# Optimization experiments

Hardware: AMD Instinct MI355X
Metric: run time of the kernel (lower is better)

The kernel has to match this reference:

```python
import jax, jax.numpy as jnp
import numpy as np

B, L, D_IN = 2, 4096, 512
H, D_K, D_V, D_OUT = 8, 64, 64, 512


def setup_inputs() -> dict:
    key = jax.random.key(0)
    k0, k1, k2, k3, k4 = jax.random.split(key, 5)
    x = jax.random.normal(k0, (B, L, D_IN), dtype=jnp.float32)
    W_q = jax.random.uniform(k1, (H, D_IN, D_K), dtype=jnp.float32)
    W_k = jax.random.uniform(k2, (H, D_IN, D_K), dtype=jnp.float32)
    W_v = jax.random.uniform(k3, (H, D_IN, D_V), dtype=jnp.float32)
    W_o = jax.random.uniform(k4, (H, D_V, D_OUT), dtype=jnp.float32)
    return {"x": x, "W_q": W_q, "W_k": W_k, "W_v": W_v, "W_o": W_o}


def reference(x, W_q, W_k, W_v, W_o):
    # x: (b, l, d_in); projections per head -> (b, h, l, d)
    Q = jnp.einsum('hjk,blj->bhlk', W_q, x)
    K = jnp.einsum('hjk,blj->bhlk', W_k, x)
    V = jnp.einsum('hjv,blj->bhlv', W_v, x)
    # no softmax: pure bilinear attention (Q K^T) V
    scores = jnp.einsum('bhik,bhjk->bhij', Q, K)          # (b, h, l, l)
    values = jnp.einsum('bhqk,bhkv->bhqv', scores, V)     # (b, h, l, d_v)
    return jnp.einsum('hvo,bhlv->blo', W_o, values)       # (b, l, d_out)
```

## Files before the change

kernel.cpp:

```cpp
#include <hip/hip_runtime.h>
#include <cstdint>


#define BDIM 2
#define LDIM 4096
#define DIN 512
#define HDIM 8
#define DK 64
#define DV 64
#define DOUT 512
#define NS 16

using bf16_t = __bf16;
typedef __bf16 bf16x8 __attribute__((ext_vector_type(8)));
typedef float floatx4 __attribute__((ext_vector_type(4)));

__device__ __forceinline__ unsigned short f2bf(float f) {
    unsigned int u = __builtin_bit_cast(unsigned int, f);
    u += 0x7FFFu + ((u >> 16) & 1u);
    return (unsigned short)(u >> 16);
}

__device__ __forceinline__ void gld_lds16(const void* g, void* l) {
    __builtin_amdgcn_global_load_lds(
        (const __attribute__((address_space(1))) void*)g,
        (__attribute__((address_space(3))) void*)l, 16, 0, 0);
}

template <int BM, int BN, bool TRANS_OUT, int OUT_MODE>
__device__ __forceinline__ void gemm_core(const bf16_t* A, const bf16_t* B,
                                          void* Cp, int K, int lda, int ldb,
                                          int ldc, int tm, int tn) {
    constexpr int BK = 32;
    constexpr int WM = BM / 2, WN = BN / 2;
    constexpr int FM = WM / 16, FN = WN / 16;
    __shared__ bf16_t As[BM * BK];
    __shared__ bf16_t Bs[BN * BK];
    const int tid = threadIdx.x;
    const int lane = tid & 63;
    const int wr = (tid >> 7) & 1;
    const int wc = (tid >> 6) & 1;

    A += (size_t)tm * lda;
    B += (size_t)tn * ldb;

    floatx4 acc[FM][FN] = {};

    for (int k0 = 0; k0 < K; k0 += BK) {
#pragma unroll
        for (int i = 0; i < (BM * 4) / 256; ++i) {
            int c = i * 256 + tid;
            int m = c >> 2, kc = c & 3;
            gld_lds16(A + (size_t)m * lda + k0 + kc * 8, As + c * 8);
        }
#pragma unroll
        for (int i = 0; i < (BN * 4) / 256; ++i) {
            int c = i * 256 + tid;
            int m = c >> 2, kc = c & 3;
            gld_lds16(B + (size_t)m * ldb + k0 + kc * 8, Bs + c * 8);
        }
        __syncthreads();

        bf16x8 aF[FM], bF[FN];
#pragma unroll
        for (int fm = 0; fm < FM; ++fm)
            aF[fm] = *(const bf16x8*)(As + (wr * WM + fm * 16 + (lane & 15)) * BK +
                                      (lane >> 4) * 8);
#pragma unroll
        for (int fn = 0; fn < FN; ++fn)
            bF[fn] = *(const bf16x8*)(Bs + (wc * WN + fn * 16 + (lane & 15)) * BK +
                                      (lane >> 4) * 8);
#pragma unroll
        for (int fm = 0; fm < FM; ++fm)
#pragma unroll
            for (int fn = 0; fn < FN; ++fn)
                acc[fm][fn] = __builtin_amdgcn_mfma_f32_16x16x32_bf16(
                    aF[fm], bF[fn], acc[fm][fn], 0, 0, 0);
        __syncthreads();
    }

    const int cr4 = (lane >> 4) * 4;
    const int cn = lane & 15;
#pragma unroll
    for (int fm = 0; fm < FM; ++fm)
#pragma unroll
        for (int fn = 0; fn < FN; ++fn)
#pragma unroll
            for (int r = 0; r < 4; ++r) {
                int m = tm + wr * WM + fm * 16 + cr4 + r;
                int n = tn + wc * WN + fn * 16 + cn;
                size_t idx = TRANS_OUT ? ((size_t)n * ldc + m)
                                       : ((size_t)m * ldc + n);
                if (OUT_MODE == 0)
                    ((float*)Cp)[idx] = acc[fm][fn][r];
                else
                    ((unsigned short*)Cp)[idx] = f2bf(acc[fm][fn][r]);
            }
}

__global__ __launch_bounds__(256) void k_gram(const bf16_t* xT, float* Gp) {
    int z = blockIdx.z, b = z / NS, s = z % NS;
    const bf16_t* Ab = xT + (size_t)b * DIN * LDIM + s * (LDIM / NS);
    gemm_core<128, 128, false, 0>(Ab, Ab, Gp + (size_t)z * DIN * DIN,
                                  LDIM / NS, LDIM, LDIM, DIN,
                                  blockIdx.x * 128, blockIdx.y * 128);
}

__global__ __launch_bounds__(256) void k_gred(const float* Gp, unsigned short* G16) {
    size_t idx = ((size_t)blockIdx.x * 256 + threadIdx.x) * 4;
    int b = (int)(idx >> 18);
    size_t r = idx & (((size_t)1 << 18) - 1);
    float4 s = make_float4(0.f, 0.f, 0.f, 0.f);
#pragma unroll
    for (int sl = 0; sl < NS; ++sl) {
        float4 v = *(const float4*)(Gp + (((size_t)(b * NS + sl)) << 18) + r);
        s.x += v.x; s.y += v.y; s.z += v.z; s.w += v.w;
    }
    *(ushort4*)(G16 + idx) =
        make_ushort4(f2bf(s.x), f2bf(s.y), f2bf(s.z), f2bf(s.w));
}

__global__ __launch_bounds__(256) void k_proj(const bf16_t* G16, const bf16_t* WvT,
                                              unsigned short* UT) {
    int b = blockIdx.z;
    gemm_core<64, 64, true, 1>(G16 + (size_t)b * DIN * DIN, WvT,
                               UT + (size_t)b * DIN * DIN, DIN, DIN, DIN, DIN,
                               blockIdx.x * 64, blockIdx.y * 64);
}

__global__ __launch_bounds__(256) void k_kvnw(const bf16_t* WkT, const bf16_t* UT,
                                              const bf16_t* WoT, unsigned short* NT) {
    int b = blockIdx.x >> 3, h = blockIdx.x & 7;
    __shared__ bf16_t As[64 * 32];
    __shared__ bf16_t Bs[64 * 32];
    __shared__ bf16_t Ms[64 * 64];
    __shared__ bf16_t Aw[64 * 64];
    const int tid = threadIdx.x;
    const int lane = tid & 63;
    const int wr = (tid >> 7) & 1, wc = (tid >> 6) & 1;
    const int cr4 = (lane >> 4) * 4, cn = lane & 15;

    const bf16_t* A = WkT + (size_t)h * DK * DIN;
    const bf16_t* B = UT + (size_t)b * DIN * DIN + (size_t)h * DV * DIN;
    floatx4 acc[2][2] = {};
    for (int k0 = 0; k0 < DIN; k0 += 32) {
        int c = tid, m = c >> 2, kc = c & 3;
        gld_lds16(A + (size_t)m * DIN + k0 + kc * 8, As + c * 8);
        gld_lds16(B + (size_t)m * DIN + k0 + kc * 8, Bs + c * 8);
        __syncthreads();
        bf16x8 aF[2], bF[2];
#pragma unroll
        for (int f = 0; f < 2; ++f) {
            aF[f] = *(const bf16x8*)(As + (wr * 32 + f * 16 + cn) * 32 + (lane >> 4) * 8);
            bF[f] = *(const bf16x8*)(Bs + (wc * 32 + f * 16 + cn) * 32 + (lane >> 4) * 8);
        }
#pragma unroll
        for (int fm = 0; fm < 2; ++fm)
#pragma unroll
            for (int fn = 0; fn < 2; ++fn)
                acc[fm][fn] = __builtin_amdgcn_mfma_f32_16x16x32_bf16(
                    aF[fm], bF[fn], acc[fm][fn], 0, 0, 0);
        __syncthreads();
    }
#pragma unroll
    for (int fm = 0; fm < 2; ++fm)
#pragma unroll
        for (int fn = 0; fn < 2; ++fn)
#pragma unroll
            for (int r = 0; r < 4; ++r) {
                int m = wr * 32 + fm * 16 + cr4 + r;
                int n = wc * 32 + fn * 16 + cn;
                ((unsigned short*)Ms)[m * 64 + n] = f2bf(acc[fm][fn][r]);
            }
    __syncthreads();

    const bf16_t* Ao = WoT + (size_t)h * DOUT * DV;
    unsigned short* NTb = NT + (size_t)b * DOUT * DIN + h * DK;
    for (int mo = 0; mo < 8; ++mo) {
        floatx4 a2[2][2] = {};
#pragma unroll
        for (int i = 0; i < 2; ++i) {
            int c = i * 256 + tid, m = c >> 3, kc = c & 7;
            gld_lds16(Ao + (size_t)(mo * 64 + m) * DV + kc * 8, Aw + c * 8);
        }
        __syncthreads();
#pragma unroll
        for (int k0 = 0; k0 < 64; k0 += 32) {
            bf16x8 aF[2], bF[2];
#pragma unroll
            for (int f = 0; f < 2; ++f) {
                aF[f] = *(const bf16x8*)(Aw + (wr * 32 + f * 16 + cn) * 64 + k0 + (lane >> 4) * 8);
                bF[f] = *(const bf16x8*)(Ms + (wc * 32 + f * 16 + cn) * 64 + k0 + (lane >> 4) * 8);
            }
#pragma unroll
            for (int fm = 0; fm < 2; ++fm)
#pragma unroll
                for (int fn = 0; fn < 2; ++fn)
                    a2[fm][fn] = __builtin_amdgcn_mfma_f32_16x16x32_bf16(
                        aF[fm], bF[fn], a2[fm][fn], 0, 0, 0);
        }
#pragma unroll
        for (int fm = 0; fm < 2; ++fm)
#pragma unroll
            for (int fn = 0; fn < 2; ++fn)
#pragma unroll
                for (int r = 0; r < 4; ++r) {
                    int m = wr * 32 + fm * 16 + cr4 + r;
                    int n = wc * 32 + fn * 16 + cn;
                    NTb[(size_t)(mo * 64 + m) * DIN + n] = f2bf(a2[fm][fn][r]);
                }
        __syncthreads();
    }
}

__global__ __launch_bounds__(256) void k_cw(const bf16_t* Wq_cat, const bf16_t* NT,
                                            unsigned short* CT) {
    int b = blockIdx.z;
    gemm_core<64, 64, true, 1>(Wq_cat, NT + (size_t)b * DOUT * DIN,
                               CT + (size_t)b * DIN * DOUT, DIN, DIN, DIN, DIN,
                               blockIdx.x * 64, blockIdx.y * 64);
}

__global__ __launch_bounds__(256) void k_out(const bf16_t* x16, const bf16_t* CT,
                                             float* out) {
    int b = blockIdx.z;
    gemm_core<128, 128, false, 0>(x16 + (size_t)b * LDIM * DIN,
                                  CT + (size_t)b * DIN * DOUT,
                                  out + (size_t)b * LDIM * DOUT, DIN, DIN, DIN,
                                  DOUT, blockIdx.x * 128, blockIdx.y * 128);
}

__global__ __launch_bounds__(256) void k_convx(const float* x, unsigned short* xb,
                                               unsigned short* xT) {
    __shared__ unsigned short T[64][65];
    int b = blockIdx.z, l0 = blockIdx.y * 64, d0 = blockIdx.x * 64;
    int tr = threadIdx.x >> 4, tc4 = (threadIdx.x & 15) * 4;
    const float* xp = x + (size_t)b * LDIM * DIN;
    unsigned short* xbp = xb + (size_t)b * LDIM * DIN;
#pragma unroll
    for (int p = 0; p < 4; ++p) {
        int l = p * 16 + tr;
        float4 v = *(const float4*)(xp + (size_t)(l0 + l) * DIN + d0 + tc4);
        unsigned short q0 = f2bf(v.x), q1 = f2bf(v.y), q2 = f2bf(v.z), q3 = f2bf(v.w);
        *(ushort4*)(xbp + (size_t)(l0 + l) * DIN + d0 + tc4) =
            make_ushort4(q0, q1, q2, q3);
        T[l][tc4 + 0] = q0; T[l][tc4 + 1] = q1;
        T[l][tc4 + 2] = q2; T[l][tc4 + 3] = q3;
    }
    __syncthreads();
    unsigned short* xTp = xT + (size_t)b * DIN * LDIM;
#pragma unroll
    for (int p = 0; p < 4; ++p) {
        int d = p * 16 + tr;
        ushort4 u = make_ushort4(T[tc4 + 0][d], T[tc4 + 1][d], T[tc4 + 2][d],
                                 T[tc4 + 3][d]);
        *(ushort4*)(xTp + (size_t)(d0 + d) * LDIM + l0 + tc4) = u;
    }
}

__global__ __launch_bounds__(256) void k_prep(const float* Wq, const float* Wk,
                                              const float* Wv, const float* Wo,
                                              unsigned short* WqC, unsigned short* WkT,
                                              unsigned short* WvT, unsigned short* WoT) {
    __shared__ unsigned short T[64][65];
    int t = blockIdx.x, job = blockIdx.y, h = blockIdx.z;
    int tr = threadIdx.x >> 4, tc4 = (threadIdx.x & 15) * 4;
    if (job == 0) {
        const float* src = Wq + (size_t)h * DIN * DK;
#pragma unroll
        for (int p = 0; p < 4; ++p) {
            int i = t * 64 + p * 16 + tr;
            float4 v = *(const float4*)(src + (size_t)i * DK + tc4);
            *(ushort4*)(WqC + (size_t)i * (HDIM * DK) + h * DK + tc4) =
                make_ushort4(f2bf(v.x), f2bf(v.y), f2bf(v.z), f2bf(v.w));
        }
        return;
    }
    const float* src;
    unsigned short* dst;
    int rows, cols, r0, c0;
    if (job == 1) {
        src = Wk + (size_t)h * DIN * DK; dst = WkT + (size_t)h * DK * DIN;
        rows = DIN; cols = DK; r0 = t * 64; c0 = 0;
    } else if (job == 2) {
        src = Wv + (size_t)h * DIN * DV; dst = WvT + (size_t)h * DV * DIN;
        rows = DIN; cols = DV; r0 = t * 64; c0 = 0;
    } else {
        src = Wo + (size_t)h * DV * DOUT; dst = WoT + (size_t)h * DOUT * DV;
        rows = DV; cols = DOUT; r0 = 0; c0 = t * 64;
    }
#pragma unroll
    for (int p = 0; p < 4; ++p) {
        int r = p * 16 + tr;
        float4 v = *(const float4*)(src + (size_t)(r0 + r) * cols + c0 + tc4);
        T[r][tc4 + 0] = f2bf(v.x); T[r][tc4 + 1] = f2bf(v.y);
        T[r][tc4 + 2] = f2bf(v.z); T[r][tc4 + 3] = f2bf(v.w);
    }
    __syncthreads();
#pragma unroll
    for (int p = 0; p < 4; ++p) {
        int c = p * 16 + tr;
        ushort4 u = make_ushort4(T[tc4 + 0][c], T[tc4 + 1][c], T[tc4 + 2][c],
                                 T[tc4 + 3][c]);
        *(ushort4*)(dst + (size_t)(c0 + c) * rows + r0 + tc4) = u;
    }
}

extern "C" void kernel_launch(void* const* d_in, const int* in_sizes, int n_in,
                              void* d_out, int out_size, void* d_ws, size_t ws_size,
                              hipStream_t stream) {
    const float* x  = (const float*)d_in[0];
    const float* Wq = (const float*)d_in[1];
    const float* Wk = (const float*)d_in[2];
    const float* Wv = (const float*)d_in[3];
    const float* Wo = (const float*)d_in[4];
    float* out = (float*)d_out;

    unsigned short* w = (unsigned short*)d_ws;
    unsigned short* xb16  = w; w += (size_t)BDIM * LDIM * DIN;
    unsigned short* xT16  = w; w += (size_t)BDIM * DIN * LDIM;
    unsigned short* WqC   = w; w += (size_t)DIN * HDIM * DK;
    unsigned short* WkT   = w; w += (size_t)HDIM * DK * DIN;
    unsigned short* WvT   = w; w += (size_t)HDIM * DV * DIN;
    unsigned short* WoT   = w; w += (size_t)HDIM * DOUT * DV;
    unsigned short* G16   = w; w += (size_t)BDIM * DIN * DIN;
    unsigned short* UT    = w; w += (size_t)BDIM * DIN * DIN;
    unsigned short* NT    = w; w += (size_t)BDIM * DOUT * DIN;
    unsigned short* CT    = w; w += (size_t)BDIM * DIN * DOUT;
    float* Gp = (float*)(((uintptr_t)w + 255) & ~(uintptr_t)255);

    k_prep<<<dim3(8, 4, HDIM), 256, 0, stream>>>(Wq, Wk, Wv, Wo, WqC, WkT, WvT, WoT);
    k_convx<<<dim3(DIN / 64, LDIM / 64, BDIM), 256, 0, stream>>>(x, xb16, xT16);

    k_gram<<<dim3(4, 4, BDIM * NS), 256, 0, stream>>>((const bf16_t*)xT16, Gp);
    k_gred<<<dim3((BDIM * DIN * DIN) / 1024), 256, 0, stream>>>(Gp, G16);
    k_proj<<<dim3(8, 8, BDIM), 256, 0, stream>>>((const bf16_t*)G16,
                                                 (const bf16_t*)WvT, UT);
    k_kvnw<<<dim3(BDIM * HDIM), 256, 0, stream>>>((const bf16_t*)WkT,
                                                  (const bf16_t*)UT,
                                                  (const bf16_t*)WoT, NT);
    k_cw<<<dim3(8, 8, BDIM), 256, 0, stream>>>((const bf16_t*)WqC,
                                               (const bf16_t*)NT, CT);
    k_out<<<dim3(LDIM / 128, DOUT / 128, BDIM), 256, 0, stream>>>(
        (const bf16_t*)xb16, (const bf16_t*)CT, out);
}
```

Before: 142.2 us.

## Fuse prep kernels, split kvnw across output tiles, widen BK, halve Gram split-K

```diff
diff --git a/kernel.cpp b/kernel.cpp
--- a/kernel.cpp
+++ b/kernel.cpp
@@ -9,7 +9,7 @@
 #define DK 64
 #define DV 64
 #define DOUT 512
-#define NS 16
+#define NS 8
 
 using bf16_t = __bf16;
 typedef __bf16 bf16x8 __attribute__((ext_vector_type(8)));
@@ -27,13 +27,13 @@
         (__attribute__((address_space(3))) void*)l, 16, 0, 0);
 }
 
-template <int BM, int BN, bool TRANS_OUT, int OUT_MODE>
+template <int BM, int BN, int BK, bool TRANS_OUT, int OUT_MODE>
 __device__ __forceinline__ void gemm_core(const bf16_t* A, const bf16_t* B,
                                           void* Cp, int K, int lda, int ldb,
                                           int ldc, int tm, int tn) {
-    constexpr int BK = 32;
     constexpr int WM = BM / 2, WN = BN / 2;
     constexpr int FM = WM / 16, FN = WN / 16;
+    constexpr int CPR = BK / 8;
     __shared__ bf16_t As[BM * BK];
     __shared__ bf16_t Bs[BN * BK];
     const int tid = threadIdx.x;
@@ -48,34 +48,37 @@
 
     for (int k0 = 0; k0 < K; k0 += BK) {
 #pragma unroll
-        for (int i = 0; i < (BM * 4) / 256; ++i) {
+        for (int i = 0; i < (BM * CPR) / 256; ++i) {
             int c = i * 256 + tid;
-            int m = c >> 2, kc = c & 3;
+            int m = c / CPR, kc = c % CPR;
             gld_lds16(A + (size_t)m * lda + k0 + kc * 8, As + c * 8);
         }
 #pragma unroll
-        for (int i = 0; i < (BN * 4) / 256; ++i) {
+        for (int i = 0; i < (BN * CPR) / 256; ++i) {
             int c = i * 256 + tid;
-            int m = c >> 2, kc = c & 3;
+            int m = c / CPR, kc = c % CPR;
             gld_lds16(B + (size_t)m * ldb + k0 + kc * 8, Bs + c * 8);
         }
         __syncthreads();
 
-        bf16x8 aF[FM], bF[FN];
-#pragma unroll
-        for (int fm = 0; fm < FM; ++fm)
-            aF[fm] = *(const bf16x8*)(As + (wr * WM + fm * 16 + (lane & 15)) * BK +
-                                      (lane >> 4) * 8);
-#pragma unroll
-        for (int fn = 0; fn < FN; ++fn)
-            bF[fn] = *(const bf16x8*)(Bs + (wc * WN + fn * 16 + (lane & 15)) * BK +
-                                      (lane >> 4) * 8);
-#pragma unroll
-        for (int fm = 0; fm < FM; ++fm)
+#pragma unroll
+        for (int kk = 0; kk < BK; kk += 32) {
+            bf16x8 aF[FM], bF[FN];
+#pragma unroll
+            for (int fm = 0; fm < FM; ++fm)
+                aF[fm] = *(const bf16x8*)(As + (wr * WM + fm * 16 + (lane & 15)) * BK +
+                                          kk + (lane >> 4) * 8);
 #pragma unroll
             for (int fn = 0; fn < FN; ++fn)
-                acc[fm][fn] = __builtin_amdgcn_mfma_f32_16x16x32_bf16(
-                    aF[fm], bF[fn], acc[fm][fn], 0, 0, 0);
+                bF[fn] = *(const bf16x8*)(Bs + (wc * WN + fn * 16 + (lane & 15)) * BK +
+                                          kk + (lane >> 4) * 8);
+#pragma unroll
+            for (int fm = 0; fm < FM; ++fm)
+#pragma unroll
+                for (int fn = 0; fn < FN; ++fn)
+                    acc[fm][fn] = __builtin_amdgcn_mfma_f32_16x16x32_bf16(
+                        aF[fm], bF[fn], acc[fm][fn], 0, 0, 0);
+        }
         __syncthreads();
     }
 
@@ -101,9 +104,9 @@
 __global__ __launch_bounds__(256) void k_gram(const bf16_t* xT, float* Gp) {
     int z = blockIdx.z, b = z / NS, s = z % NS;
     const bf16_t* Ab = xT + (size_t)b * DIN * LDIM + s * (LDIM / NS);
-    gemm_core<128, 128, false, 0>(Ab, Ab, Gp + (size_t)z * DIN * DIN,
-                                  LDIM / NS, LDIM, LDIM, DIN,
-                                  blockIdx.x * 128, blockIdx.y * 128);
+    gemm_core<128, 128, 64, false, 0>(Ab, Ab, Gp + (size_t)z * DIN * DIN,
+                                      LDIM / NS, LDIM, LDIM, DIN,
+                                      blockIdx.x * 128, blockIdx.y * 128);
 }
 
 __global__ __launch_bounds__(256) void k_gred(const float* Gp, unsigned short* G16) {
@@ -123,14 +126,15 @@
 __global__ __launch_bounds__(256) void k_proj(const bf16_t* G16, const bf16_t* WvT,
                                               unsigned short* UT) {
     int b = blockIdx.z;
-    gemm_core<64, 64, true, 1>(G16 + (size_t)b * DIN * DIN, WvT,
-                               UT + (size_t)b * DIN * DIN, DIN, DIN, DIN, DIN,
-                               blockIdx.x * 64, blockIdx.y * 64);
+    gemm_core<64, 64, 32, true, 1>(G16 + (size_t)b * DIN * DIN, WvT,
+                                   UT + (size_t)b * DIN * DIN, DIN, DIN, DIN,
+                                   DIN, blockIdx.x * 64, blockIdx.y * 64);
 }
 
 __global__ __launch_bounds__(256) void k_kvnw(const bf16_t* WkT, const bf16_t* UT,
                                               const bf16_t* WoT, unsigned short* NT) {
-    int b = blockIdx.x >> 3, h = blockIdx.x & 7;
+    int mo = blockIdx.x;
+    int b = blockIdx.y >> 3, h = blockIdx.y & 7;
     __shared__ bf16_t As[64 * 32];
     __shared__ bf16_t Bs[64 * 32];
     __shared__ bf16_t Ms[64 * 64];
@@ -172,99 +176,98 @@
                 int n = wc * 32 + fn * 16 + cn;
                 ((unsigned short*)Ms)[m * 64 + n] = f2bf(acc[fm][fn][r]);
             }
-    __syncthreads();
 
     const bf16_t* Ao = WoT + (size_t)h * DOUT * DV;
     unsigned short* NTb = NT + (size_t)b * DOUT * DIN + h * DK;
-    for (int mo = 0; mo < 8; ++mo) {
-        floatx4 a2[2][2] = {};
-#pragma unroll
-        for (int i = 0; i < 2; ++i) {
-            int c = i * 256 + tid, m = c >> 3, kc = c & 7;
-            gld_lds16(Ao + (size_t)(mo * 64 + m) * DV + kc * 8, Aw + c * 8);
-        }
-        __syncthreads();
-#pragma unroll
-        for (int k0 = 0; k0 < 64; k0 += 32) {
-            bf16x8 aF[2], bF[2];
-#pragma unroll
-            for (int f = 0; f < 2; ++f) {
-                aF[f] = *(const bf16x8*)(Aw + (wr * 32 + f * 16 + cn) * 64 + k0 + (lane >> 4) * 8);
-                bF[f] = *(const bf16x8*)(Ms + (wc * 32 + f * 16 + cn) * 64 + k0 + (lane >> 4) * 8);
+#pragma unroll
+    for (int i = 0; i < 2; ++i) {
+        int c = i * 256 + tid, m = c >> 3, kc = c & 7;
+        gld_lds16(Ao + (size_t)(mo * 64 + m) * DV + kc * 8, Aw + c * 8);
+    }
+    __syncthreads();
+    floatx4 a2[2][2] = {};
+#pragma unroll
+    for (int k0 = 0; k0 < 64; k0 += 32) {
+        bf16x8 aF[2], bF[2];
+#pragma unroll
+        for (int f = 0; f < 2; ++f) {
+            aF[f] = *(const bf16x8*)(Aw + (wr * 32 + f * 16 + cn) * 64 + k0 + (lane >> 4) * 8);
+            bF[f] = *(const bf16x8*)(Ms + (wc * 32 + f * 16 + cn) * 64 + k0 + (lane >> 4) * 8);
+        }
+#pragma unroll
+        for (int fm = 0; fm < 2; ++fm)
+#pragma unroll
+            for (int fn = 0; fn < 2; ++fn)
+                a2[fm][fn] = __builtin_amdgcn_mfma_f32_16x16x32_bf16(
+                    aF[fm], bF[fn], a2[fm][fn], 0, 0, 0);
+    }
+#pragma unroll
+    for (int fm = 0; fm < 2; ++fm)
+#pragma unroll
+        for (int fn = 0; fn < 2; ++fn)
+#pragma unroll
+            for (int r = 0; r < 4; ++r) {
+                int m = wr * 32 + fm * 16 + cr4 + r;
+                int n = wc * 32 + fn * 16 + cn;
+                NTb[(size_t)(mo * 64 + m) * DIN + n] = f2bf(a2[fm][fn][r]);
             }
-#pragma unroll
-            for (int fm = 0; fm < 2; ++fm)
-#pragma unroll
-                for (int fn = 0; fn < 2; ++fn)
-                    a2[fm][fn] = __builtin_amdgcn_mfma_f32_16x16x32_bf16(
-                        aF[fm], bF[fn], a2[fm][fn], 0, 0, 0);
-        }
-#pragma unroll
-        for (int fm = 0; fm < 2; ++fm)
-#pragma unroll
-            for (int fn = 0; fn < 2; ++fn)
-#pragma unroll
-                for (int r = 0; r < 4; ++r) {
-                    int m = wr * 32 + fm * 16 + cr4 + r;
-                    int n = wc * 32 + fn * 16 + cn;
-                    NTb[(size_t)(mo * 64 + m) * DIN + n] = f2bf(a2[fm][fn][r]);
-                }
-        __syncthreads();
-    }
 }
 
 __global__ __launch_bounds__(256) void k_cw(const bf16_t* Wq_cat, const bf16_t* NT,
                                             unsigned short* CT) {
     int b = blockIdx.z;
-    gemm_core<64, 64, true, 1>(Wq_cat, NT + (size_t)b * DOUT * DIN,
-                               CT + (size_t)b * DIN * DOUT, DIN, DIN, DIN, DIN,
-                               blockIdx.x * 64, blockIdx.y * 64);
+    gemm_core<64, 64, 32, true, 1>(Wq_cat, NT + (size_t)b * DOUT * DIN,
+                                   CT + (size_t)b * DIN * DOUT, DIN, DIN, DIN,
+                                   DIN, blockIdx.x * 64, blockIdx.y * 64);
 }
 
 __global__ __launch_bounds__(256) void k_out(const bf16_t* x16, const bf16_t* CT,
                                              float* out) {
     int b = blockIdx.z;
-    gemm_core<128, 128, false, 0>(x16 + (size_t)b * LDIM * DIN,
-                                  CT + (size_t)b * DIN * DOUT,
-                                  out + (size_t)b * LDIM * DOUT, DIN, DIN, DIN,
-                                  DOUT, blockIdx.x * 128, blockIdx.y * 128);
-}
-
-__global__ __launch_bounds__(256) void k_convx(const float* x, unsigned short* xb,
-                                               unsigned short* xT) {
+    gemm_core<128, 128, 64, false, 0>(x16 + (size_t)b * LDIM * DIN,
+                                      CT + (size_t)b * DIN * DOUT,
+                                      out + (size_t)b * LDIM * DOUT, DIN, DIN,
+                                      DIN, DOUT, blockIdx.x * 128,
+                                      blockIdx.y * 128);
+}
+
+__global__ __launch_bounds__(256) void k_prep2(
+    const float* x, const float* Wq, const float* Wk, const float* Wv,
+    const float* Wo, unsigned short* xb, unsigned short* xT,
+    unsigned short* WqC, unsigned short* WkT, unsigned short* WvT,
+    unsigned short* WoT) {
     __shared__ unsigned short T[64][65];
-    int b = blockIdx.z, l0 = blockIdx.y * 64, d0 = blockIdx.x * 64;
     int tr = threadIdx.x >> 4, tc4 = (threadIdx.x & 15) * 4;
-    const float* xp = x + (size_t)b * LDIM * DIN;
-    unsigned short* xbp = xb + (size_t)b * LDIM * DIN;
-#pragma unroll
-    for (int p = 0; p < 4; ++p) {
-        int l = p * 16 + tr;
-        float4 v = *(const float4*)(xp + (size_t)(l0 + l) * DIN + d0 + tc4);
-        unsigned short q0 = f2bf(v.x), q1 = f2bf(v.y), q2 = f2bf(v.z), q3 = f2bf(v.w);
-        *(ushort4*)(xbp + (size_t)(l0 + l) * DIN + d0 + tc4) =
-            make_ushort4(q0, q1, q2, q3);
-        T[l][tc4 + 0] = q0; T[l][tc4 + 1] = q1;
-        T[l][tc4 + 2] = q2; T[l][tc4 + 3] = q3;
-    }
-    __syncthreads();
-    unsigned short* xTp = xT + (size_t)b * DIN * LDIM;
-#pragma unroll
-    for (int p = 0; p < 4; ++p) {
-        int d = p * 16 + tr;
-        ushort4 u = make_ushort4(T[tc4 + 0][d], T[tc4 + 1][d], T[tc4 + 2][d],
-                                 T[tc4 + 3][d]);
-        *(ushort4*)(xTp + (size_t)(d0 + d) * LDIM + l0 + tc4) = u;
-    }
-}
-
-__global__ __launch_bounds__(256) void k_prep(const float* Wq, const float* Wk,
-                                              const float* Wv, const float* Wo,
-                                              unsigned short* WqC, unsigned short* WkT,
-                                              unsigned short* WvT, unsigned short* WoT) {
-    __shared__ unsigned short T[64][65];
-    int t = blockIdx.x, job = blockIdx.y, h = blockIdx.z;
-    int tr = threadIdx.x >> 4, tc4 = (threadIdx.x & 15) * 4;
+    int bid = blockIdx.x;
+    if (bid < 1024) {
+        int b = bid >> 9, r = bid & 511;
+        int d0 = (r & 7) * 64, l0 = (r >> 3) * 64;
+        const float* xp = x + (size_t)b * LDIM * DIN;
+        unsigned short* xbp = xb + (size_t)b * LDIM * DIN;
+#pragma unroll
+        for (int p = 0; p < 4; ++p) {
+            int l = p * 16 + tr;
+            float4 v = *(const float4*)(xp + (size_t)(l0 + l) * DIN + d0 + tc4);
+            unsigned short q0 = f2bf(v.x), q1 = f2bf(v.y), q2 = f2bf(v.z),
+                           q3 = f2bf(v.w);
+            *(ushort4*)(xbp + (size_t)(l0 + l) * DIN + d0 + tc4) =
+                make_ushort4(q0, q1, q2, q3);
+            T[l][tc4 + 0] = q0; T[l][tc4 + 1] = q1;
+            T[l][tc4 + 2] = q2; T[l][tc4 + 3] = q3;
+        }
+        __syncthreads();
+        unsigned short* xTp = xT + (size_t)b * DIN * LDIM;
+#pragma unroll
+        for (int p = 0; p < 4; ++p) {
+            int d = p * 16 + tr;
+            ushort4 u = make_ushort4(T[tc4 + 0][d], T[tc4 + 1][d], T[tc4 + 2][d],
+                                     T[tc4 + 3][d]);
+            *(ushort4*)(xTp + (size_t)(d0 + d) * LDIM + l0 + tc4) = u;
+        }
+        return;
+    }
+    int p_ = bid - 1024;
+    int t = p_ & 7, job = (p_ >> 3) & 3, h = p_ >> 5;
     if (job == 0) {
         const float* src = Wq + (size_t)h * DIN * DK;
 #pragma unroll
@@ -329,16 +332,15 @@
     unsigned short* CT    = w; w += (size_t)BDIM * DIN * DOUT;
     float* Gp = (float*)(((uintptr_t)w + 255) & ~(uintptr_t)255);
 
-    k_prep<<<dim3(8, 4, HDIM), 256, 0, stream>>>(Wq, Wk, Wv, Wo, WqC, WkT, WvT, WoT);
-    k_convx<<<dim3(DIN / 64, LDIM / 64, BDIM), 256, 0, stream>>>(x, xb16, xT16);
-
+    k_prep2<<<dim3(1280), 256, 0, stream>>>(x, Wq, Wk, Wv, Wo, xb16, xT16,
+                                            WqC, WkT, WvT, WoT);
     k_gram<<<dim3(4, 4, BDIM * NS), 256, 0, stream>>>((const bf16_t*)xT16, Gp);
     k_gred<<<dim3((BDIM * DIN * DIN) / 1024), 256, 0, stream>>>(Gp, G16);
     k_proj<<<dim3(8, 8, BDIM), 256, 0, stream>>>((const bf16_t*)G16,
                                                  (const bf16_t*)WvT, UT);
-    k_kvnw<<<dim3(BDIM * HDIM), 256, 0, stream>>>((const bf16_t*)WkT,
-                                                  (const bf16_t*)UT,
-                                                  (const bf16_t*)WoT, NT);
+    k_kvnw<<<dim3(8, BDIM * HDIM), 256, 0, stream>>>((const bf16_t*)WkT,
+                                                     (const bf16_t*)UT,
+                                                     (const bf16_t*)WoT, NT);
     k_cw<<<dim3(8, 8, BDIM), 256, 0, stream>>>((const bf16_t*)WqC,
                                                (const bf16_t*)NT, CT);
     k_out<<<dim3(LDIM / 128, DOUT / 128, BDIM), 256, 0, stream>>>(
```

Result: faster. 133.5 us (-6.2%).
